# Performance work log

Measured on AMD Instinct MI355X. Metric: run time of the kernel, lower is better.

Reference implementation:

```python
import jax, jax.numpy as jnp
import numpy as np

# NF4 (NormalFloat4) codebook from QLoRA / bitsandbytes
NF4_TABLE = jnp.array([
    -1.0, -0.6961928009986877, -0.5250730514526367, -0.39491748809814453,
    -0.28444138169288635, -0.18477343022823334, -0.09105003625154495, 0.0,
    0.07958029955625534, 0.16093020141124725, 0.24611230194568634,
    0.33791524171829224, 0.44070982933044434, 0.5626170039176941,
    0.7229568362236023, 1.0], dtype=jnp.float32)

IN_FEATURES = 4096
OUT_FEATURES = 11008
BLOCKSIZE = 64
NUMEL = IN_FEATURES * OUT_FEATURES          # 45_088_768
PACKED = NUMEL // 2                          # 22_544_384
NBLOCKS = NUMEL // BLOCKSIZE                 # 704_512


def setup_inputs() -> dict:
    key = jax.random.key(0)
    k1, k2, k3, k4 = jax.random.split(key, 4)
    x = jax.random.normal(k1, (2048, IN_FEATURES), dtype=jnp.float32)
    # packed uint8 codes, stored as int32 in [0, 256)
    packed = jax.random.randint(k2, (PACKED,), 0, 256, dtype=jnp.int32)
    # per-block absmax scales (positive)
    absmax = jax.random.uniform(k3, (NBLOCKS,), dtype=jnp.float32, minval=0.01, maxval=1.0)
    bias = jax.random.normal(k4, (OUT_FEATURES,), dtype=jnp.float32)
    return {"x": x, "packed": packed, "absmax": absmax, "bias": bias}


def _dequantize_nf4(packed, absmax):
    # unpack two 4-bit codes per byte: high nibble first, then low nibble
    hi = packed >> 4            # [P]
    lo = packed & 0xF           # [P]
    codes = jnp.stack([hi, lo], axis=-1).reshape(-1)       # [numel]
    vals = jnp.take(NF4_TABLE, codes)                      # [numel]
    # per-block absmax scaling
    w = (vals.reshape(-1, BLOCKSIZE) * absmax[:, None]).reshape(OUT_FEATURES, IN_FEATURES)
    return w


def reference(x, packed, absmax, bias):
    w = _dequantize_nf4(packed, absmax)                    # [out, in]
    # y = x @ W^T + b
    return jnp.einsum('ti,oi->to', x, w) + bias[None, :]
```

## Files before the change

kernel.cpp:

```cpp
#include <hip/hip_runtime.h>
#include <hip/hip_bf16.h>


#define IN_F   4096
#define OUT_F  11008
#define M_ROWS 2048
#define BM 128
#define BN 128
#define BK 64
#define LDSS 72

typedef short  s16x8 __attribute__((ext_vector_type(8)));
typedef unsigned short u16x8 __attribute__((ext_vector_type(8)));
typedef float  f32x4 __attribute__((ext_vector_type(4)));

__device__ const float NF4_C[16] = {
    -1.0f, -0.6961928009986877f, -0.5250730514526367f, -0.39491748809814453f,
    -0.28444138169288635f, -0.18477343022823334f, -0.09105003625154495f, 0.0f,
    0.07958029955625534f, 0.16093020141124725f, 0.24611230194568634f,
    0.33791524171829224f, 0.44070982933044434f, 0.5626170039176941f,
    0.7229568362236023f, 1.0f};

static __device__ __forceinline__ unsigned short f2bf(float f) {
    union { float f; unsigned int u; } c;
    c.f = f;
    unsigned int u = c.u;
    u += 0x7fffu + ((u >> 16) & 1u);
    return (unsigned short)(u >> 16);
}

static __device__ __forceinline__ void gload_lds16(const void* g, void* l) {
    __builtin_amdgcn_global_load_lds(
        (const __attribute__((address_space(1))) void*)g,
        (__attribute__((address_space(3))) void*)l, 16, 0, 0);
}

__global__ __launch_bounds__(256)
void convert_x_kernel(const float* __restrict__ x, unsigned short* __restrict__ xb) {
    const size_t t = (size_t)blockIdx.x * 256 + threadIdx.x;
    const float4* src = reinterpret_cast<const float4*>(x) + t * 2;
    float4 v0 = src[0];
    float4 v1 = src[1];
    u16x8 o;
    o[0] = f2bf(v0.x); o[1] = f2bf(v0.y); o[2] = f2bf(v0.z); o[3] = f2bf(v0.w);
    o[4] = f2bf(v1.x); o[5] = f2bf(v1.y); o[6] = f2bf(v1.z); o[7] = f2bf(v1.w);
    *reinterpret_cast<u16x8*>(xb + t * 8) = o;
}

__global__ __launch_bounds__(256)
void dequant_w_kernel(const int* __restrict__ packed, const float* __restrict__ absmax,
                      unsigned short* __restrict__ wb) {
    __shared__ float2 tab[256];
    tab[threadIdx.x] = make_float2(NF4_C[threadIdx.x >> 4], NF4_C[threadIdx.x & 15]);
    __syncthreads();

    const size_t t = (size_t)blockIdx.x * 256 + threadIdx.x;
    const int4* p = reinterpret_cast<const int4*>(packed) + t * 2;
    int4 a = p[0];
    int4 b = p[1];
    const float s = absmax[t >> 2];

    int vs[8] = {a.x, a.y, a.z, a.w, b.x, b.y, b.z, b.w};
    unsigned int ow[8];
#pragma unroll
    for (int j = 0; j < 8; ++j) {
        float2 tv = tab[vs[j] & 0xFF];
        ow[j] = (unsigned int)f2bf(tv.x * s) | ((unsigned int)f2bf(tv.y * s) << 16);
    }
    uint4* dst = reinterpret_cast<uint4*>(wb + t * 16);
    dst[0] = make_uint4(ow[0], ow[1], ow[2], ow[3]);
    dst[1] = make_uint4(ow[4], ow[5], ow[6], ow[7]);
}

__global__ __launch_bounds__(256, 2)
void gemm_bt_kernel(const unsigned short* __restrict__ xb,
                    const unsigned short* __restrict__ wb,
                    const float* __restrict__ bias,
                    float* __restrict__ out) {
    __shared__ __align__(16) unsigned short As[BM * BK];
    __shared__ __align__(16) unsigned short Bs[BN * BK];

    const int tid  = threadIdx.x;
    const int lane = tid & 63;
    const int wave = tid >> 6;
    const int quad = lane >> 4;
    const int l16  = lane & 15;
    const int wm = wave & 1;
    const int wn = wave >> 1;

    const int mBase = blockIdx.y * BM;
    const int nBase = blockIdx.x * BN;

    const int srow = tid >> 3;
    const int scol = (tid & 7) * 8;

    f32x4 acc[4][4];
#pragma unroll
    for (int mi = 0; mi < 4; ++mi)
#pragma unroll
        for (int ni = 0; ni < 4; ++ni)
            acc[mi][ni] = (f32x4){0.f, 0.f, 0.f, 0.f};

    const unsigned short* aSrc = xb + (size_t)(mBase + srow) * IN_F + scol;
    const unsigned short* bSrc = wb + (size_t)(nBase + srow) * IN_F + scol;

    for (int kt = 0; kt < IN_F / BK; ++kt) {
        const int k0 = kt * BK;
        __syncthreads();
#pragma unroll
        for (int i = 0; i < 4; ++i)
            gload_lds16(aSrc + (size_t)i * 32 * IN_F + k0, &As[(i * 32 + srow) * BK + scol]);
#pragma unroll
        for (int i = 0; i < 4; ++i)
            gload_lds16(bSrc + (size_t)i * 32 * IN_F + k0, &Bs[(i * 32 + srow) * BK + scol]);
        __syncthreads();

#pragma unroll
        for (int kk = 0; kk < 2; ++kk) {
            const int kof = kk * 32 + quad * 8;
            s16x8 af[4], bfr[4];
#pragma unroll
            for (int mi = 0; mi < 4; ++mi)
                af[mi] = *reinterpret_cast<const s16x8*>(
                    &As[(wm * 64 + mi * 16 + l16) * BK + kof]);
#pragma unroll
            for (int ni = 0; ni < 4; ++ni)
                bfr[ni] = *reinterpret_cast<const s16x8*>(
                    &Bs[(wn * 64 + ni * 16 + l16) * BK + kof]);
#pragma unroll
            for (int mi = 0; mi < 4; ++mi)
#pragma unroll
                for (int ni = 0; ni < 4; ++ni)
                    acc[mi][ni] = __builtin_amdgcn_mfma_f32_16x16x32_bf16(
                        af[mi], bfr[ni], acc[mi][ni], 0, 0, 0);
        }
    }

    float bv[4];
#pragma unroll
    for (int ni = 0; ni < 4; ++ni)
        bv[ni] = bias[nBase + wn * 64 + ni * 16 + l16];
#pragma unroll
    for (int mi = 0; mi < 4; ++mi) {
        const int rbase = mBase + wm * 64 + mi * 16 + quad * 4;
#pragma unroll
        for (int ni = 0; ni < 4; ++ni) {
            const int col = nBase + wn * 64 + ni * 16 + l16;
#pragma unroll
            for (int r = 0; r < 4; ++r)
                out[(size_t)(rbase + r) * OUT_F + col] = acc[mi][ni][r] + bv[ni];
        }
    }
}

__global__ __launch_bounds__(256, 2)
void nf4_linear_fused(const float* __restrict__ x,
                      const int* __restrict__ packed,
                      const float* __restrict__ absmax,
                      const float* __restrict__ bias,
                      float* __restrict__ out) {
    __shared__ __align__(16) unsigned short As[BM * LDSS];
    __shared__ __align__(16) unsigned short Bs[BN * LDSS];
    __shared__ float2 tab[256];

    const int tid  = threadIdx.x;
    const int lane = tid & 63;
    const int wave = tid >> 6;
    const int quad = lane >> 4;
    const int l16  = lane & 15;
    const int wm = wave & 1;
    const int wn = wave >> 1;
    const int mBase = blockIdx.y * BM;
    const int nBase = blockIdx.x * BN;

    tab[tid] = make_float2(NF4_C[tid >> 4], NF4_C[tid & 15]);

    f32x4 acc[4][4];
#pragma unroll
    for (int mi = 0; mi < 4; ++mi)
#pragma unroll
        for (int ni = 0; ni < 4; ++ni)
            acc[mi][ni] = (f32x4){0.f, 0.f, 0.f, 0.f};

    const int brow  = tid >> 1;
    const int bhalf = tid & 1;
    const int ng    = nBase + brow;

    for (int kt = 0; kt < IN_F / BK; ++kt) {
        const int k0 = kt * BK;
        __syncthreads();
#pragma unroll
        for (int i = 0; i < 4; ++i) {
            int gid = tid + i * 256;
            int row = gid >> 3;
            int c8  = gid & 7;
            const float4* src = reinterpret_cast<const float4*>(
                x + (size_t)(mBase + row) * IN_F + k0 + c8 * 8);
            float4 v0 = src[0];
            float4 v1 = src[1];
            u16x8 o;
            o[0] = f2bf(v0.x); o[1] = f2bf(v0.y); o[2] = f2bf(v0.z); o[3] = f2bf(v0.w);
            o[4] = f2bf(v1.x); o[5] = f2bf(v1.y); o[6] = f2bf(v1.z); o[7] = f2bf(v1.w);
            *reinterpret_cast<u16x8*>(&As[row * LDSS + c8 * 8]) = o;
        }
        {
            const float scale = absmax[(size_t)ng * 64 + (k0 >> 6)];
            const int4* bp = reinterpret_cast<const int4*>(
                packed + (size_t)ng * (IN_F / 2) + (k0 >> 1) + bhalf * 16);
            const int colw = bhalf * 32;
#pragma unroll
            for (int c = 0; c < 4; ++c) {
                int4 v = bp[c];
                int vs[4] = {v.x, v.y, v.z, v.w};
                unsigned int ow[4];
#pragma unroll
                for (int j = 0; j < 4; ++j) {
                    float2 t = tab[vs[j] & 0xFF];
                    ow[j] = (unsigned int)f2bf(t.x * scale)
                          | ((unsigned int)f2bf(t.y * scale) << 16);
                }
                *reinterpret_cast<uint4*>(&Bs[brow * LDSS + colw + c * 8]) =
                    *reinterpret_cast<const uint4*>(ow);
            }
        }
        __syncthreads();

#pragma unroll
        for (int kk = 0; kk < 2; ++kk) {
            const int kof = kk * 32 + quad * 8;
            s16x8 af[4], bfr[4];
#pragma unroll
            for (int mi = 0; mi < 4; ++mi)
                af[mi] = *reinterpret_cast<const s16x8*>(
                    &As[(wm * 64 + mi * 16 + l16) * LDSS + kof]);
#pragma unroll
            for (int ni = 0; ni < 4; ++ni)
                bfr[ni] = *reinterpret_cast<const s16x8*>(
                    &Bs[(wn * 64 + ni * 16 + l16) * LDSS + kof]);
#pragma unroll
            for (int mi = 0; mi < 4; ++mi)
#pragma unroll
                for (int ni = 0; ni < 4; ++ni)
                    acc[mi][ni] = __builtin_amdgcn_mfma_f32_16x16x32_bf16(
                        af[mi], bfr[ni], acc[mi][ni], 0, 0, 0);
        }
    }

    float bv[4];
#pragma unroll
    for (int ni = 0; ni < 4; ++ni)
        bv[ni] = bias[nBase + wn * 64 + ni * 16 + l16];
#pragma unroll
    for (int mi = 0; mi < 4; ++mi) {
        const int rbase = mBase + wm * 64 + mi * 16 + quad * 4;
#pragma unroll
        for (int ni = 0; ni < 4; ++ni) {
            const int col = nBase + wn * 64 + ni * 16 + l16;
#pragma unroll
            for (int r = 0; r < 4; ++r)
                out[(size_t)(rbase + r) * OUT_F + col] = acc[mi][ni][r] + bv[ni];
        }
    }
}

extern "C" void kernel_launch(void* const* d_in, const int* in_sizes, int n_in,
                              void* d_out, int out_size, void* d_ws, size_t ws_size,
                              hipStream_t stream) {
    const float* x      = (const float*)d_in[0];
    const int*   packed = (const int*)d_in[1];
    const float* absmax = (const float*)d_in[2];
    const float* bias   = (const float*)d_in[3];
    float* out = (float*)d_out;

    const size_t xb_bytes = (size_t)M_ROWS * IN_F * 2;
    const size_t wb_bytes = (size_t)OUT_F * IN_F * 2;
    if (ws_size >= xb_bytes + wb_bytes) {
        unsigned short* xb = (unsigned short*)d_ws;
        unsigned short* wb = (unsigned short*)((char*)d_ws + xb_bytes);
        convert_x_kernel<<<dim3((M_ROWS * IN_F) / (256 * 8)), dim3(256), 0, stream>>>(x, xb);
        dequant_w_kernel<<<dim3((OUT_F * IN_F / 2) / (256 * 8)), dim3(256), 0, stream>>>(
            packed, absmax, wb);
        gemm_bt_kernel<<<dim3(OUT_F / BN, M_ROWS / BM), dim3(256), 0, stream>>>(
            xb, wb, bias, out);
    } else {
        nf4_linear_fused<<<dim3(OUT_F / BN, M_ROWS / BM), dim3(256), 0, stream>>>(
            x, packed, absmax, bias, out);
    }
}
```

Before: 431.1 us.

## Merge prep kernels, swap GEMM grid order, use nontemporal loads and stores

Combines the x-to-bf16 conversion and the NF4 weight dequantization into one prep kernel, split by block index, which removes one launch and lets the two run concurrently. Swaps the GEMM grid axes so consecutive blocks walk along M for the same N tile. This changes which operands get reused in L2: W tiles are shared and x tiles are re-read. Uses nontemporal loads for the streamed inputs and nontemporal stores for the output to reduce cache pollution, at the risk of hurting L2 reuse of xb/wb written by the prep step.

New measurement: 396.2 us. 1.09x faster.

```diff
diff --git a/kernel.cpp b/kernel.cpp
--- a/kernel.cpp
+++ b/kernel.cpp
@@ -13,6 +13,8 @@
 typedef short  s16x8 __attribute__((ext_vector_type(8)));
 typedef unsigned short u16x8 __attribute__((ext_vector_type(8)));
 typedef float  f32x4 __attribute__((ext_vector_type(4)));
+typedef int    i32x4 __attribute__((ext_vector_type(4)));
+typedef unsigned int u32x4 __attribute__((ext_vector_type(4)));
 
 __device__ const float NF4_C[16] = {
     -1.0f, -0.6961928009986877f, -0.5250730514526367f, -0.39491748809814453f,
@@ -35,41 +37,46 @@
         (__attribute__((address_space(3))) void*)l, 16, 0, 0);
 }
 
+#define DQ_BLOCKS 11008
+#define CV_BLOCKS 4096
+
 __global__ __launch_bounds__(256)
-void convert_x_kernel(const float* __restrict__ x, unsigned short* __restrict__ xb) {
-    const size_t t = (size_t)blockIdx.x * 256 + threadIdx.x;
-    const float4* src = reinterpret_cast<const float4*>(x) + t * 2;
-    float4 v0 = src[0];
-    float4 v1 = src[1];
-    u16x8 o;
-    o[0] = f2bf(v0.x); o[1] = f2bf(v0.y); o[2] = f2bf(v0.z); o[3] = f2bf(v0.w);
-    o[4] = f2bf(v1.x); o[5] = f2bf(v1.y); o[6] = f2bf(v1.z); o[7] = f2bf(v1.w);
-    *reinterpret_cast<u16x8*>(xb + t * 8) = o;
-}
-
-__global__ __launch_bounds__(256)
-void dequant_w_kernel(const int* __restrict__ packed, const float* __restrict__ absmax,
-                      unsigned short* __restrict__ wb) {
-    __shared__ float2 tab[256];
-    tab[threadIdx.x] = make_float2(NF4_C[threadIdx.x >> 4], NF4_C[threadIdx.x & 15]);
-    __syncthreads();
-
-    const size_t t = (size_t)blockIdx.x * 256 + threadIdx.x;
-    const int4* p = reinterpret_cast<const int4*>(packed) + t * 2;
-    int4 a = p[0];
-    int4 b = p[1];
-    const float s = absmax[t >> 2];
-
-    int vs[8] = {a.x, a.y, a.z, a.w, b.x, b.y, b.z, b.w};
-    unsigned int ow[8];
-#pragma unroll
-    for (int j = 0; j < 8; ++j) {
-        float2 tv = tab[vs[j] & 0xFF];
-        ow[j] = (unsigned int)f2bf(tv.x * s) | ((unsigned int)f2bf(tv.y * s) << 16);
-    }
-    uint4* dst = reinterpret_cast<uint4*>(wb + t * 16);
-    dst[0] = make_uint4(ow[0], ow[1], ow[2], ow[3]);
-    dst[1] = make_uint4(ow[4], ow[5], ow[6], ow[7]);
+void prep_kernel(const float* __restrict__ x,
+                 const int* __restrict__ packed,
+                 const float* __restrict__ absmax,
+                 unsigned short* __restrict__ xb,
+                 unsigned short* __restrict__ wb) {
+    if (blockIdx.x < DQ_BLOCKS) {
+        __shared__ float2 tab[256];
+        tab[threadIdx.x] = make_float2(NF4_C[threadIdx.x >> 4], NF4_C[threadIdx.x & 15]);
+        __syncthreads();
+
+        const size_t t = (size_t)blockIdx.x * 256 + threadIdx.x;
+        const i32x4* p = reinterpret_cast<const i32x4*>(packed) + t * 2;
+        i32x4 a = __builtin_nontemporal_load(p);
+        i32x4 b = __builtin_nontemporal_load(p + 1);
+        const float s = absmax[t >> 2];
+
+        int vs[8] = {a[0], a[1], a[2], a[3], b[0], b[1], b[2], b[3]};
+        unsigned int ow[8];
+#pragma unroll
+        for (int j = 0; j < 8; ++j) {
+            float2 tv = tab[vs[j] & 0xFF];
+            ow[j] = (unsigned int)f2bf(tv.x * s) | ((unsigned int)f2bf(tv.y * s) << 16);
+        }
+        u32x4* dst = reinterpret_cast<u32x4*>(wb + t * 16);
+        dst[0] = (u32x4){ow[0], ow[1], ow[2], ow[3]};
+        dst[1] = (u32x4){ow[4], ow[5], ow[6], ow[7]};
+    } else {
+        const size_t t = (size_t)(blockIdx.x - DQ_BLOCKS) * 256 + threadIdx.x;
+        const f32x4* src = reinterpret_cast<const f32x4*>(x) + t * 2;
+        f32x4 v0 = __builtin_nontemporal_load(src);
+        f32x4 v1 = __builtin_nontemporal_load(src + 1);
+        u16x8 o;
+        o[0] = f2bf(v0[0]); o[1] = f2bf(v0[1]); o[2] = f2bf(v0[2]); o[3] = f2bf(v0[3]);
+        o[4] = f2bf(v1[0]); o[5] = f2bf(v1[1]); o[6] = f2bf(v1[2]); o[7] = f2bf(v1[3]);
+        *reinterpret_cast<u16x8*>(xb + t * 8) = o;
+    }
 }
 
 __global__ __launch_bounds__(256, 2)
@@ -88,8 +95,8 @@
     const int wm = wave & 1;
     const int wn = wave >> 1;
 
-    const int mBase = blockIdx.y * BM;
-    const int nBase = blockIdx.x * BN;
+    const int mBase = blockIdx.x * BM;
+    const int nBase = blockIdx.y * BN;
 
     const int srow = tid >> 3;
     const int scol = (tid & 7) * 8;
@@ -148,7 +155,8 @@
             const int col = nBase + wn * 64 + ni * 16 + l16;
 #pragma unroll
             for (int r = 0; r < 4; ++r)
-                out[(size_t)(rbase + r) * OUT_F + col] = acc[mi][ni][r] + bv[ni];
+                __builtin_nontemporal_store(acc[mi][ni][r] + bv[ni],
+                    &out[(size_t)(rbase + r) * OUT_F + col]);
         }
     }
 }
@@ -277,10 +285,9 @@
     if (ws_size >= xb_bytes + wb_bytes) {
         unsigned short* xb = (unsigned short*)d_ws;
         unsigned short* wb = (unsigned short*)((char*)d_ws + xb_bytes);
-        convert_x_kernel<<<dim3((M_ROWS * IN_F) / (256 * 8)), dim3(256), 0, stream>>>(x, xb);
-        dequant_w_kernel<<<dim3((OUT_F * IN_F / 2) / (256 * 8)), dim3(256), 0, stream>>>(
-            packed, absmax, wb);
-        gemm_bt_kernel<<<dim3(OUT_F / BN, M_ROWS / BM), dim3(256), 0, stream>>>(
+        prep_kernel<<<dim3(DQ_BLOCKS + CV_BLOCKS), dim3(256), 0, stream>>>(
+            x, packed, absmax, xb, wb);
+        gemm_bt_kernel<<<dim3(M_ROWS / BM, OUT_F / BN), dim3(256), 0, stream>>>(
             xb, wb, bias, out);
     } else {
         nf4_linear_fused<<<dim3(OUT_F / BN, M_ROWS / BM), dim3(256), 0, stream>>>(
```
